# Performance work log

Measured on AMD Instinct MI355X. Metric: run time of the kernel, lower is better.

Reference implementation:

```python
import jax, jax.numpy as jnp
import numpy as np

FM = 256          # feature_maps
ROUNDS = 32
N_VARS = 4000
N_CLAUSES = 16800 # ~4.2 * n_vars (3-SAT phase transition)
K = 3             # literals per clause
EPS = 1e-8


def setup_inputs() -> dict:
    key = jax.random.key(0)
    ks = jax.random.split(key, 20)

    def nrm(k, shape):
        # tf.initializers.RandomNormal default stddev = 0.05
        return jax.random.normal(k, shape, jnp.float32) * 0.05

    vs = jax.random.randint(ks[0], (N_CLAUSES, K), 1, N_VARS + 1)
    sg = jnp.where(jax.random.uniform(ks[1], (N_CLAUSES, K)) < 0.5, -1, 1)
    return {
        "clause_lits": (vs * sg).astype(jnp.int32),  # signed 1-based literals
        "n_vars": N_VARS,
        "L_init": nrm(ks[2], (1, FM)), "C_init": nrm(ks[3], (1, FM)),
        "LC_W0": nrm(ks[4], (FM, FM)), "LC_b0": jnp.zeros((FM,), jnp.float32),
        "LC_W1": nrm(ks[5], (FM, FM)), "LC_b1": jnp.zeros((FM,), jnp.float32),
        "LC_W2": nrm(ks[6], (FM, FM)), "LC_b2": jnp.zeros((FM,), jnp.float32),
        "CL_W0": nrm(ks[7], (FM, FM)), "CL_b0": jnp.zeros((FM,), jnp.float32),
        "CL_W1": nrm(ks[8], (FM, FM)), "CL_b1": jnp.zeros((FM,), jnp.float32),
        "CL_W2": nrm(ks[9], (FM, FM)), "CL_b2": jnp.zeros((FM,), jnp.float32),
        "C_Wx": nrm(ks[10], (FM, 4 * FM)), "C_Wh": nrm(ks[11], (FM, 4 * FM)),
        "C_b": jnp.zeros((4 * FM,), jnp.float32),
        "L_Wx": nrm(ks[12], (2 * FM, 4 * FM)), "L_Wh": nrm(ks[13], (FM, 4 * FM)),
        "L_b": jnp.zeros((4 * FM,), jnp.float32),
        "V_W0": nrm(ks[14], (2 * FM, 2 * FM)), "V_b0": jnp.zeros((2 * FM,), jnp.float32),
        "V_W1": nrm(ks[15], (2 * FM, 2 * FM)), "V_b1": jnp.zeros((2 * FM,), jnp.float32),
        "V_W2": nrm(ks[16], (2 * FM, 1)), "V_b2": jnp.zeros((1,), jnp.float32),
    }


def _mlp3(x, W0, b0, W1, b1, W2, b2):
    h = jax.nn.relu(x @ W0 + b0)
    h = jax.nn.relu(h @ W1 + b1)
    return h @ W2 + b2


def _lstm(x, h, c, Wx, Wh, b):
    # keras LSTMCell: gate order i, f, g, o; sigmoid recurrent, tanh activation
    z = x @ Wx + h @ Wh + b
    i, f, g, o = jnp.split(z, 4, axis=1)
    c = jax.nn.sigmoid(f) * c + jax.nn.sigmoid(i) * jnp.tanh(g)
    h = jax.nn.sigmoid(o) * jnp.tanh(c)
    return h, c


def reference(clause_lits, n_vars, L_init, C_init,
              LC_W0, LC_b0, LC_W1, LC_b1, LC_W2, LC_b2,
              CL_W0, CL_b0, CL_W1, CL_b1, CL_W2, CL_b2,
              C_Wx, C_Wh, C_b, L_Wx, L_Wh, L_b,
              V_W0, V_b0, V_W1, V_b1, V_W2, V_b2):
    n_clauses = clause_lits.shape[0]
    n_lits = 2 * n_vars
    lits = clause_lits.reshape(-1)                         # [E]
    sign = jnp.sign(lits).astype(jnp.float32)              # [E]
    var_idx = jnp.abs(lits) - 1                            # [E] 0-based var
    lit_idx = jnp.where(lits > 0, var_idx, n_vars + var_idx)
    clause_idx = jnp.repeat(jnp.arange(n_clauses), clause_lits.shape[1])

    denom = jnp.sqrt(jnp.float32(FM))
    l_h = jnp.tile(L_init / denom, (n_lits, 1))
    c_h = jnp.tile(C_init / denom, (n_clauses, 1))
    l_c = jnp.zeros_like(l_h)
    c_c = jnp.zeros_like(c_h)

    def vote(lh):
        variables = jnp.concatenate([lh[:n_vars], lh[n_vars:]], axis=1)  # [n_vars, 2*FM]
        return _mlp3(variables, V_W0, V_b0, V_W1, V_b1, V_W2, V_b2)      # [n_vars, 1]

    def clause_loss(logits):
        # softplus_log_square_loss: clause_val = exp(-sum_lit softplus(sign*logit))
        vals = logits[var_idx, 0] * sign                   # [E]
        s = jax.ops.segment_sum(jax.nn.softplus(vals), clause_idx,
                                num_segments=n_clauses, indices_are_sorted=True)
        cv = jnp.exp(-s)
        return jnp.sum(jnp.square(-jnp.log(1.0 - cv + EPS)))

    def round_fn(carry, _):
        lh, lc, ch, cc, loss = carry
        lc_pre = _mlp3(lh, LC_W0, LC_b0, LC_W1, LC_b1, LC_W2, LC_b2)
        # SpMM adj^T @ msgs: scatter literal messages into clauses
        lc_msgs = jax.ops.segment_sum(lc_pre[lit_idx], clause_idx,
                                      num_segments=n_clauses, indices_are_sorted=True)
        ch, cc = _lstm(lc_msgs, ch, cc, C_Wx, C_Wh, C_b)
        cl_pre = _mlp3(ch, CL_W0, CL_b0, CL_W1, CL_b1, CL_W2, CL_b2)
        # SpMM adj @ msgs: scatter clause messages into literals
        cl_msgs = jax.ops.segment_sum(cl_pre[clause_idx], lit_idx, num_segments=n_lits)
        flipped = jnp.concatenate([lh[n_vars:], lh[:n_vars]], axis=0)
        lh, lc = _lstm(jnp.concatenate([cl_msgs, flipped], axis=1), lh, lc,
                       L_Wx, L_Wh, L_b)
        loss = loss + clause_loss(vote(lh))
        return (lh, lc, ch, cc, loss), None

    (l_h, l_c, c_h, c_c, loss), _ = jax.lax.scan(
        round_fn, (l_h, l_c, c_h, c_c, jnp.float32(0.0)), None, length=ROUNDS)
    logits = vote(l_h)
    return logits, loss / jnp.float32(ROUNDS)
```

## Files before the change

### kernel.cpp

```cpp
#include <hip/hip_runtime.h>
#include <hip/hip_bf16.h>

#define NV 4000
#define NL 8000
#define NC 16800
#define NE 50400
#define FM 256
#define ROUNDS 32

typedef short s16x8 __attribute__((ext_vector_type(8)));
typedef __bf16 b16x8 __attribute__((ext_vector_type(8)));
typedef float f32x4 __attribute__((ext_vector_type(4)));
union V8 { s16x8 s; b16x8 b; ushort u[8]; };

using gaddr_t = const void __attribute__((address_space(1)))*;
using laddr_t = void __attribute__((address_space(3)))*;

__device__ __forceinline__ float b2f(ushort u) {
    union { uint i; float f; } v; v.i = ((uint)u) << 16; return v.f;
}
__device__ __forceinline__ ushort f2b(float f) {
    __hip_bfloat16 h = __float2bfloat16(f);
    return *(ushort*)&h;
}

__global__ void zero_kernel(float* __restrict__ p, int n) {
    int i = blockIdx.x * blockDim.x + threadIdx.x;
    if (i < n) p[i] = 0.0f;
}
__global__ void f2b_kernel(const float* __restrict__ src, ushort* __restrict__ dst, int n) {
    int i = blockIdx.x * blockDim.x + threadIdx.x;
    if (i < n) dst[i] = f2b(src[i]);
}
__global__ void transpose_w_kernel(const float* __restrict__ in, ushort* __restrict__ out,
                                   int K, int N, int ldo, int koff, int perm) {
    int idx = blockIdx.x * blockDim.x + threadIdx.x;
    if (idx >= K * N) return;
    int n = idx / K, k = idx - n * K;
    int row = perm ? ((n & 255) * 4 + (n >> 8)) : n;
    out[(size_t)row * ldo + koff + k] = f2b(in[(size_t)k * N + n]);
}
__global__ void permute_bias_kernel(const float* __restrict__ b, float* __restrict__ bp) {
    int n = blockIdx.x * blockDim.x + threadIdx.x;
    if (n < 1024) bp[(n & 255) * 4 + (n >> 8)] = b[n];
}

__global__ void init_lh_kernel(const float* __restrict__ Li, ushort* __restrict__ lh,
                               ushort* __restrict__ lhflip) {
    int idx = blockIdx.x * blockDim.x + threadIdx.x;
    if (idx < NL * FM) {
        ushort v = f2b(Li[idx & (FM - 1)] * (1.0f / 16.0f));
        lh[idx] = v; lhflip[idx] = v;
    }
}
__global__ void init_ch_kernel(const float* __restrict__ Ci, ushort* __restrict__ ch) {
    int idx = blockIdx.x * blockDim.x + threadIdx.x;
    if (idx < NC * FM) ch[idx] = f2b(Ci[idx & (FM - 1)] * (1.0f / 16.0f));
}

__global__ void csr_count_kernel(const int* __restrict__ lits, int* __restrict__ deg) {
    int e = blockIdx.x * blockDim.x + threadIdx.x;
    if (e >= NE) return;
    int l = lits[e];
    int v = (l > 0 ? l : -l) - 1;
    int li = (l > 0) ? v : NV + v;
    atomicAdd(&deg[li], 1);
}
__global__ void csr_scan_kernel(const int* __restrict__ deg, int* __restrict__ rowptr,
                                int* __restrict__ nxt) {
    if (threadIdx.x == 0 && blockIdx.x == 0) {
        int acc = 0;
        for (int i = 0; i < NL; ++i) { rowptr[i] = acc; nxt[i] = acc; acc += deg[i]; }
        rowptr[NL] = acc;
    }
}
__global__ void csr_fill_kernel(const int* __restrict__ lits, int* __restrict__ nxt,
                                int* __restrict__ ecl) {
    int e = blockIdx.x * blockDim.x + threadIdx.x;
    if (e >= NE) return;
    int l = lits[e];
    int v = (l > 0 ? l : -l) - 1;
    int li = (l > 0) ? v : NV + v;
    int pos = atomicAdd(&nxt[li], 1);
    ecl[pos] = e / 3;
}

#define BKT 64

#define MLPR 32
__global__ __launch_bounds__(256) void mlp3_kernel(
    const ushort* __restrict__ A,
    const ushort* __restrict__ W0t, const float* __restrict__ b0,
    const ushort* __restrict__ W1t, const float* __restrict__ b1,
    const ushort* __restrict__ W2t, const float* __restrict__ b2,
    ushort* __restrict__ out, int M)
{
    __shared__ __align__(16) ushort As[MLPR * BKT];
    __shared__ __align__(16) ushort Wl[256 * BKT];
    __shared__ __align__(16) ushort Ab[MLPR * 264];
    const int tid = threadIdx.x;
    const int lane = tid & 63, wid = tid >> 6;
    const int rowBase = blockIdx.x * MLPR;
    const int lr = lane >> 3, ql = (lane & 7) ^ lr;
    const int cl16 = lane & 15, kg = lane >> 4;

    const ushort* Wt[3] = {W0t, W1t, W2t};
    const float*  bs[3] = {b0, b1, b2};

    #pragma unroll
    for (int layer = 0; layer < 3; ++layer) {
        f32x4 acc[2][4];
        #pragma unroll
        for (int i = 0; i < 2; ++i)
            #pragma unroll
            for (int j = 0; j < 4; ++j) acc[i][j] = (f32x4){0.f, 0.f, 0.f, 0.f};

        for (int kt = 0; kt < 4; ++kt) {
            __syncthreads();
            #pragma unroll
            for (int t = 0; t < 8; ++t) {
                int row = wid * 64 + t * 8 + lr;
                __builtin_amdgcn_global_load_lds(
                    (gaddr_t)(Wt[layer] + (size_t)row * 256 + kt * 64 + ql * 8),
                    (laddr_t)&Wl[(wid * 64 + t * 8) * BKT + lane * 8], 16, 0, 0);
            }
            if (layer == 0) {
                int row = rowBase + wid * 8 + lr;
                if (row > M - 1) row = M - 1;
                __builtin_amdgcn_global_load_lds(
                    (gaddr_t)(A + (size_t)row * 256 + kt * 64 + ql * 8),
                    (laddr_t)&As[wid * 512 + lane * 8], 16, 0, 0);
            }
            __syncthreads();
            #pragma unroll
            for (int s = 0; s < 2; ++s) {
                int kq8 = s * 4 + kg;
                V8 af[2], bf[4];
                #pragma unroll
                for (int i = 0; i < 2; ++i) {
                    int m = i * 16 + cl16;
                    if (layer == 0)
                        af[i].s = *(const s16x8*)&As[m * BKT + ((kq8 ^ (m & 7)) * 8)];
                    else
                        af[i].s = *(const s16x8*)&Ab[m * 264 + kt * 64 + kq8 * 8];
                }
                #pragma unroll
                for (int j = 0; j < 4; ++j) {
                    int n = wid * 64 + j * 16 + cl16;
                    bf[j].s = *(const s16x8*)&Wl[n * BKT + ((kq8 ^ (n & 7)) * 8)];
                }
                #pragma unroll
                for (int i = 0; i < 2; ++i)
                    #pragma unroll
                    for (int j = 0; j < 4; ++j)
                        acc[i][j] = __builtin_amdgcn_mfma_f32_16x16x32_bf16(
                            af[i].b, bf[j].b, acc[i][j], 0, 0, 0);
            }
        }
        __syncthreads();
        const int rq = (lane >> 4) * 4;
        #pragma unroll
        for (int i = 0; i < 2; ++i)
            #pragma unroll
            for (int r = 0; r < 4; ++r) {
                int row = i * 16 + rq + r;
                #pragma unroll
                for (int j = 0; j < 4; ++j) {
                    int col = wid * 64 + j * 16 + cl16;
                    float v = acc[i][j][r] + bs[layer][col];
                    if (layer < 2) {
                        Ab[row * 264 + col] = f2b(fmaxf(v, 0.0f));
                    } else {
                        int grow = rowBase + row;
                        if (grow < M) out[(size_t)grow * 256 + col] = f2b(v);
                    }
                }
            }
    }
}

__global__ __launch_bounds__(256) void gemm16_n64_kernel(
    const ushort* __restrict__ A0, int K0,
    const ushort* __restrict__ A1, int K1,
    const ushort* __restrict__ Bt, const float* __restrict__ bias,
    ushort* __restrict__ C, int M, int N, int relu)
{
    __shared__ __align__(16) ushort Al[128 * BKT];
    __shared__ __align__(16) ushort Bl[64 * BKT];
    const int Ktot = K0 + K1;
    const int tid = threadIdx.x;
    const int rowBase = blockIdx.y * 128, colBase = blockIdx.x * 64;
    const int lane = tid & 63, wid = tid >> 6;
    const int wm = (wid & 1) * 64, wn = (wid >> 1) * 32;
    const int lr = lane >> 3, ql = (lane & 7) ^ lr;

    f32x4 acc[4][2];
    #pragma unroll
    for (int i = 0; i < 4; ++i)
        #pragma unroll
        for (int j = 0; j < 2; ++j) acc[i][j] = (f32x4){0.f, 0.f, 0.f, 0.f};

    for (int k0 = 0; k0 < Ktot; k0 += BKT) {
        const ushort* As; int ks, lda;
        if (k0 < K0) { As = A0; ks = k0; lda = K0; }
        else         { As = A1; ks = k0 - K0; lda = K1; }
        __syncthreads();
        #pragma unroll
        for (int t = 0; t < 4; ++t) {
            int rloc = (wid * 4 + t) * 8 + lr;
            int ga = rowBase + rloc; if (ga > M - 1) ga = M - 1;
            __builtin_amdgcn_global_load_lds((gaddr_t)(As + (size_t)ga * lda + ks + ql * 8),
                                             (laddr_t)&Al[(wid * 4 + t) * 512], 16, 0, 0);
        }
        #pragma unroll
        for (int t = 0; t < 2; ++t) {
            int rloc = (wid * 2 + t) * 8 + lr;
            __builtin_amdgcn_global_load_lds((gaddr_t)(Bt + (size_t)(colBase + rloc) * Ktot + k0 + ql * 8),
                                             (laddr_t)&Bl[(wid * 2 + t) * 512], 16, 0, 0);
        }
        __syncthreads();
        const int cl = lane & 15, kg = lane >> 4;
        #pragma unroll
        for (int s = 0; s < 2; ++s) {
            V8 af[4], bf[2];
            #pragma unroll
            for (int i = 0; i < 4; ++i) {
                int m = wm + i * 16 + cl;
                af[i].s = *(const s16x8*)&Al[m * BKT + (((s * 4 + kg) ^ (m & 7)) * 8)];
            }
            #pragma unroll
            for (int j = 0; j < 2; ++j) {
                int n = wn + j * 16 + cl;
                bf[j].s = *(const s16x8*)&Bl[n * BKT + (((s * 4 + kg) ^ (n & 7)) * 8)];
            }
            #pragma unroll
            for (int i = 0; i < 4; ++i)
                #pragma unroll
                for (int j = 0; j < 2; ++j)
                    acc[i][j] = __builtin_amdgcn_mfma_f32_16x16x32_bf16(af[i].b, bf[j].b,
                                                                        acc[i][j], 0, 0, 0);
        }
    }
    const int rq = (lane >> 4) * 4, cl = lane & 15;
    #pragma unroll
    for (int i = 0; i < 4; ++i)
        #pragma unroll
        for (int r = 0; r < 4; ++r) {
            int grow = rowBase + wm + i * 16 + rq + r;
            if (grow >= M) continue;
            #pragma unroll
            for (int j = 0; j < 2; ++j) {
                int gcol = colBase + wn + j * 16 + cl;
                float v = acc[i][j][r] + bias[gcol];
                if (relu) v = fmaxf(v, 0.0f);
                C[(size_t)grow * N + gcol] = f2b(v);
            }
        }
}

__global__ __launch_bounds__(256) void gemm_lstm_kernel(
    const ushort* __restrict__ A0, int K0,
    const ushort* __restrict__ A1, int K1,
    const ushort* __restrict__ A2, int K2,
    const ushort* __restrict__ Bt, const float* __restrict__ biasP,
    float* __restrict__ c32, ushort* __restrict__ h_out,
    ushort* __restrict__ hflip_out, int M)
{
    __shared__ __align__(16) ushort smem[2 * 128 * BKT];
    ushort* Al = smem;
    ushort* Bl = smem + 128 * BKT;
    const int Ktot = K0 + K1 + K2;
    const int tid = threadIdx.x;
    const int rowBase = blockIdx.y * 128, colBase = blockIdx.x * 128;
    const int lane = tid & 63, wid = tid >> 6;
    const int wm = (wid >> 1) * 64, wn = (wid & 1) * 64;
    const int lr = lane >> 3, ql = (lane & 7) ^ lr;

    f32x4 acc[4][4];
    #pragma unroll
    for (int i = 0; i < 4; ++i)
        #pragma unroll
        for (int j = 0; j < 4; ++j) acc[i][j] = (f32x4){0.f, 0.f, 0.f, 0.f};

    for (int k0 = 0; k0 < Ktot; k0 += BKT) {
        const ushort* As; int ks, lda;
        if (k0 < K0)           { As = A0; ks = k0;           lda = K0; }
        else if (k0 < K0 + K1) { As = A1; ks = k0 - K0;      lda = K1; }
        else                   { As = A2; ks = k0 - K0 - K1; lda = K2; }
        __syncthreads();
        #pragma unroll
        for (int t = 0; t < 4; ++t) {
            int rloc = (wid * 4 + t) * 8 + lr;
            int ga = rowBase + rloc; if (ga > M - 1) ga = M - 1;
            __builtin_amdgcn_global_load_lds((gaddr_t)(As + (size_t)ga * lda + ks + ql * 8),
                                             (laddr_t)&Al[(wid * 4 + t) * 512], 16, 0, 0);
            __builtin_amdgcn_global_load_lds((gaddr_t)(Bt + (size_t)(colBase + rloc) * Ktot + k0 + ql * 8),
                                             (laddr_t)&Bl[(wid * 4 + t) * 512], 16, 0, 0);
        }
        __syncthreads();
        const int cl = lane & 15, kg = lane >> 4;
        #pragma unroll
        for (int s = 0; s < 2; ++s) {
            V8 af[4], bf[4];
            #pragma unroll
            for (int i = 0; i < 4; ++i) {
                int m = wm + i * 16 + cl;
                af[i].s = *(const s16x8*)&Al[m * BKT + (((s * 4 + kg) ^ (m & 7)) * 8)];
            }
            #pragma unroll
            for (int j = 0; j < 4; ++j) {
                int n = wn + j * 16 + cl;
                bf[j].s = *(const s16x8*)&Bl[n * BKT + (((s * 4 + kg) ^ (n & 7)) * 8)];
            }
            #pragma unroll
            for (int i = 0; i < 4; ++i)
                #pragma unroll
                for (int j = 0; j < 4; ++j)
                    acc[i][j] = __builtin_amdgcn_mfma_f32_16x16x32_bf16(af[i].b, bf[j].b,
                                                                        acc[i][j], 0, 0, 0);
        }
    }
    __syncthreads();
    {
        const int rq = (lane >> 4) * 4, cl = lane & 15;
        #pragma unroll
        for (int i = 0; i < 4; ++i)
            #pragma unroll
            for (int r = 0; r < 4; ++r) {
                int rl = wm + i * 16 + rq + r;
                #pragma unroll
                for (int j = 0; j < 4; ++j) {
                    int clc = wn + j * 16 + cl;
                    smem[rl * 128 + clc] = f2b(acc[i][j][r] + biasP[colBase + clc]);
                }
            }
    }
    __syncthreads();
    const int fl = tid & 31, rg = tid >> 5;
    const int fglob = (colBase >> 2) + fl;
    #pragma unroll
    for (int k = 0; k < 16; ++k) {
        int rl = rg + 8 * k;
        int grow = rowBase + rl;
        if (grow >= M) continue;
        ushort4 g4 = *(const ushort4*)&smem[rl * 128 + fl * 4];
        float zi = b2f(g4.x), zf = b2f(g4.y), zg = b2f(g4.z), zo = b2f(g4.w);
        size_t ci = (size_t)grow * FM + fglob;
        float cold = c32[ci];
        float si = 1.0f / (1.0f + __expf(-zi));
        float sf = 1.0f / (1.0f + __expf(-zf));
        float so = 1.0f / (1.0f + __expf(-zo));
        float cn = sf * cold + si * tanhf(zg);
        float hn = so * tanhf(cn);
        c32[ci] = cn;
        ushort hb = f2b(hn);
        h_out[ci] = hb;
        if (hflip_out) hflip_out[(size_t)((grow + NV) % NL) * FM + fglob] = hb;
    }
}

__global__ void gather_lc8_kernel(const ushort* __restrict__ pre, const int* __restrict__ lits,
                                  ushort* __restrict__ out) {
    int idx = blockIdx.x * blockDim.x + threadIdx.x;
    if (idx >= NC * 32) return;
    int c = idx >> 5, f8 = (idx & 31) * 8;
    const int* cl = lits + c * 3;
    float s[8] = {};
    #pragma unroll
    for (int k = 0; k < 3; ++k) {
        int l = cl[k];
        int v = (l > 0 ? l : -l) - 1;
        int li = (l > 0) ? v : NV + v;
        V8 x; x.s = *(const s16x8*)&pre[(size_t)li * FM + f8];
        #pragma unroll
        for (int e = 0; e < 8; ++e) s[e] += b2f(x.u[e]);
    }
    V8 o;
    #pragma unroll
    for (int e = 0; e < 8; ++e) o.u[e] = f2b(s[e]);
    *(s16x8*)&out[(size_t)c * FM + f8] = o.s;
}

__global__ void gather_cl8_kernel(const ushort* __restrict__ pre, const int* __restrict__ rowptr,
                                  const int* __restrict__ ecl, ushort* __restrict__ out) {
    int idx = blockIdx.x * blockDim.x + threadIdx.x;
    if (idx >= NL * 32) return;
    int li = idx >> 5, f8 = (idx & 31) * 8;
    int j0 = rowptr[li], j1 = rowptr[li + 1];
    float s[8] = {};
    for (int j = j0; j < j1; ++j) {
        V8 x; x.s = *(const s16x8*)&pre[(size_t)ecl[j] * FM + f8];
        #pragma unroll
        for (int e = 0; e < 8; ++e) s[e] += b2f(x.u[e]);
    }
    V8 o;
    #pragma unroll
    for (int e = 0; e < 8; ++e) o.u[e] = f2b(s[e]);
    *(s16x8*)&out[(size_t)li * FM + f8] = o.s;
}

__global__ void vote_out_kernel(const ushort* __restrict__ h1, const ushort* __restrict__ w,
                                const float* __restrict__ b, float* __restrict__ logits_hist,
                                float* __restrict__ out_f32) {
    int gtid = blockIdx.x * blockDim.x + threadIdx.x;
    int wid = gtid >> 6;
    int lane = threadIdx.x & 63;
    if (wid >= NV) return;
    const ushort* hr = h1 + (size_t)wid * 512;
    float s = 0.0f;
    #pragma unroll
    for (int k = 0; k < 8; ++k) s += b2f(hr[lane + 64 * k]) * b2f(w[lane + 64 * k]);
    #pragma unroll
    for (int off = 32; off; off >>= 1) s += __shfl_down(s, off);
    if (lane == 0) {
        float v = s + b[0];
        logits_hist[wid] = v;
        out_f32[wid] = v;
    }
}

__global__ __launch_bounds__(256) void loss_all_kernel(
    const float* __restrict__ logits_hist, const int* __restrict__ lits,
    float* __restrict__ loss_arr)
{
    __shared__ float sm[256];
    const int r = blockIdx.y;
    const float* logits = logits_hist + (size_t)r * NV;
    int c = blockIdx.x * 256 + threadIdx.x;
    float t2 = 0.0f;
    if (c < NC) {
        const int* cl = lits + c * 3;
        float s = 0.0f;
        #pragma unroll
        for (int k = 0; k < 3; ++k) {
            int l = cl[k];
            int v = (l > 0 ? l : -l) - 1;
            float sg = (l > 0) ? 1.0f : -1.0f;
            float val = logits[v] * sg;
            s += fmaxf(val, 0.0f) + log1pf(__expf(-fabsf(val)));
        }
        float cv = __expf(-s);
        float t = -logf(1.0f - cv + 1e-8f);
        t2 = t * t;
    }
    sm[threadIdx.x] = t2;
    __syncthreads();
    for (int st = 128; st > 0; st >>= 1) {
        if (threadIdx.x < st) sm[threadIdx.x] += sm[threadIdx.x + st];
        __syncthreads();
    }
    if (threadIdx.x == 0) atomicAdd(&loss_arr[r], sm[0]);
}

__global__ void final_loss_kernel(const float* __restrict__ loss_arr, float* __restrict__ out) {
    if (threadIdx.x == 0 && blockIdx.x == 0) {
        float s = 0.0f;
        for (int r = 0; r < ROUNDS; ++r) s += loss_arr[r];
        out[NV] = s * (1.0f / (float)ROUNDS);
    }
}

extern "C" void kernel_launch(void* const* d_in, const int* in_sizes, int n_in,
                              void* d_out, int out_size, void* d_ws, size_t ws_size,
                              hipStream_t stream) {
    const int* lits = (const int*)d_in[0];
    float* out = (float*)d_out;

    const float* Li   = (const float*)d_in[2];
    const float* Ci   = (const float*)d_in[3];
    const float* LCW0 = (const float*)d_in[4];
    const float* LCb0 = (const float*)d_in[5];
    const float* LCW1 = (const float*)d_in[6];
    const float* LCb1 = (const float*)d_in[7];
    const float* LCW2 = (const float*)d_in[8];
    const float* LCb2 = (const float*)d_in[9];
    const float* CLW0 = (const float*)d_in[10];
    const float* CLb0 = (const float*)d_in[11];
    const float* CLW1 = (const float*)d_in[12];
    const float* CLb1 = (const float*)d_in[13];
    const float* CLW2 = (const float*)d_in[14];
    const float* CLb2 = (const float*)d_in[15];
    const float* CWx  = (const float*)d_in[16];
    const float* CWh  = (const float*)d_in[17];
    const float* Cb   = (const float*)d_in[18];
    const float* LWx  = (const float*)d_in[19];
    const float* LWh  = (const float*)d_in[20];
    const float* Lb   = (const float*)d_in[21];
    const float* VW0  = (const float*)d_in[22];
    const float* Vb0  = (const float*)d_in[23];
    const float* VW1  = (const float*)d_in[24];
    const float* Vb1  = (const float*)d_in[25];
    const float* VW2  = (const float*)d_in[26];
    const float* Vb2  = (const float*)d_in[27];
    (void)in_sizes; (void)n_in; (void)out_size; (void)ws_size;

    char* base = (char*)d_ws;
    size_t off = 0;
    auto allocB = [&](size_t bytes) {
        void* p = base + off;
        off += (bytes + 15) & ~(size_t)15;
        return p;
    };
    float*  loss_arr    = (float*)allocB(ROUNDS * 4);
    float*  logits_hist = (float*)allocB((size_t)ROUNDS * NV * 4);
    float*  lc32        = (float*)allocB((size_t)NL * FM * 4);
    float*  cc32        = (float*)allocB((size_t)NC * FM * 4);
    float*  Cb_p        = (float*)allocB(1024 * 4);
    float*  Lb_p        = (float*)allocB(1024 * 4);
    int*    deg         = (int*)allocB(NL * 4);
    int*    rowptr      = (int*)allocB((NL + 1) * 4);
    int*    nxt         = (int*)allocB(NL * 4);
    int*    ecl         = (int*)allocB(NE * 4);
    ushort* LC0t = (ushort*)allocB((size_t)256 * 256 * 2);
    ushort* LC1t = (ushort*)allocB((size_t)256 * 256 * 2);
    ushort* LC2t = (ushort*)allocB((size_t)256 * 256 * 2);
    ushort* CL0t = (ushort*)allocB((size_t)256 * 256 * 2);
    ushort* CL1t = (ushort*)allocB((size_t)256 * 256 * 2);
    ushort* CL2t = (ushort*)allocB((size_t)256 * 256 * 2);
    ushort* CWt  = (ushort*)allocB((size_t)1024 * 512 * 2);
    ushort* LWt  = (ushort*)allocB((size_t)1024 * 768 * 2);
    ushort* VW0t = (ushort*)allocB((size_t)512 * 512 * 2);
    ushort* VW1t = (ushort*)allocB((size_t)512 * 512 * 2);
    ushort* vw2  = (ushort*)allocB((size_t)512 * 2);
    ushort* lh_a = (ushort*)allocB((size_t)NL * FM * 2);
    ushort* lh_b = (ushort*)allocB((size_t)NL * FM * 2);
    ushort* lf_a = (ushort*)allocB((size_t)NL * FM * 2);
    ushort* lf_b = (ushort*)allocB((size_t)NL * FM * 2);
    ushort* ch_a = (ushort*)allocB((size_t)NC * FM * 2);
    ushort* ch_b = (ushort*)allocB((size_t)NC * FM * 2);
    ushort* lcm16 = (ushort*)allocB((size_t)NC * FM * 2);
    ushort* clm16 = (ushort*)allocB((size_t)NL * FM * 2);
    ushort* tL    = (ushort*)allocB((size_t)NL * FM * 2);
    ushort* tC    = (ushort*)allocB((size_t)NC * FM * 2);
    ushort* v0    = (ushort*)allocB((size_t)NV * 512 * 2);
    ushort* v1    = (ushort*)allocB((size_t)NV * 512 * 2);

    auto tw = [&](const float* in, ushort* o, int K, int N, int ldo, int koff, int perm) {
        hipLaunchKernelGGL(transpose_w_kernel, dim3((K * N + 255) / 256), dim3(256), 0, stream,
                           in, o, K, N, ldo, koff, perm);
    };
    tw(LCW0, LC0t, 256, 256, 256, 0, 0);
    tw(LCW1, LC1t, 256, 256, 256, 0, 0);
    tw(LCW2, LC2t, 256, 256, 256, 0, 0);
    tw(CLW0, CL0t, 256, 256, 256, 0, 0);
    tw(CLW1, CL1t, 256, 256, 256, 0, 0);
    tw(CLW2, CL2t, 256, 256, 256, 0, 0);
    tw(CWx,  CWt, 256, 1024, 512, 0, 1);
    tw(CWh,  CWt, 256, 1024, 512, 256, 1);
    tw(LWx,  LWt, 512, 1024, 768, 0, 1);
    tw(LWh,  LWt, 256, 1024, 768, 512, 1);
    tw(VW0,  VW0t, 512, 512, 512, 0, 0);
    tw(VW1,  VW1t, 512, 512, 512, 0, 0);
    hipLaunchKernelGGL(f2b_kernel, dim3(2), dim3(256), 0, stream, VW2, vw2, 512);
    hipLaunchKernelGGL(permute_bias_kernel, dim3(4), dim3(256), 0, stream, Cb, Cb_p);
    hipLaunchKernelGGL(permute_bias_kernel, dim3(4), dim3(256), 0, stream, Lb, Lb_p);

    hipLaunchKernelGGL(init_lh_kernel, dim3(NL * FM / 256), dim3(256), 0, stream, Li, lh_a, lf_a);
    hipLaunchKernelGGL(init_ch_kernel, dim3(NC * FM / 256), dim3(256), 0, stream, Ci, ch_a);
    hipLaunchKernelGGL(zero_kernel, dim3(NL * FM / 256), dim3(256), 0, stream, lc32, NL * FM);
    hipLaunchKernelGGL(zero_kernel, dim3(NC * FM / 256), dim3(256), 0, stream, cc32, NC * FM);
    hipLaunchKernelGGL(zero_kernel, dim3(1), dim3(256), 0, stream, loss_arr, ROUNDS);
    hipLaunchKernelGGL(zero_kernel, dim3((NL + 255) / 256), dim3(256), 0, stream, (float*)deg, NL);
    hipLaunchKernelGGL(csr_count_kernel, dim3((NE + 255) / 256), dim3(256), 0, stream, lits, deg);
    hipLaunchKernelGGL(csr_scan_kernel, dim3(1), dim3(64), 0, stream, deg, rowptr, nxt);
    hipLaunchKernelGGL(csr_fill_kernel, dim3((NE + 255) / 256), dim3(256), 0, stream, lits, nxt, ecl);

    auto gemm64 = [&](const ushort* A0, int K0, const ushort* A1, int K1,
                      const ushort* Bt, const float* bias, ushort* C, int M, int N, int relu) {
        hipLaunchKernelGGL(gemm16_n64_kernel, dim3(N / 64, (M + 127) / 128), dim3(256), 0, stream,
                           A0, K0, A1, K1, Bt, bias, C, M, N, relu);
    };

    ushort *lh_c = lh_a, *lh_n = lh_b, *lf_c = lf_a, *lf_n = lf_b, *ch_c = ch_a, *ch_n = ch_b;

    for (int r = 0; r < ROUNDS; ++r) {
        hipLaunchKernelGGL(mlp3_kernel, dim3(NL / MLPR), dim3(256), 0, stream,
                           lh_c, LC0t, LCb0, LC1t, LCb1, LC2t, LCb2, tL, NL);
        hipLaunchKernelGGL(gather_lc8_kernel, dim3(NC * 32 / 256), dim3(256), 0, stream,
                           tL, lits, lcm16);
        hipLaunchKernelGGL(gemm_lstm_kernel, dim3(8, (NC + 127) / 128), dim3(256), 0, stream,
                           lcm16, 256, ch_c, 256, (const ushort*)0, 0,
                           CWt, Cb_p, cc32, ch_n, (ushort*)0, NC);
        hipLaunchKernelGGL(mlp3_kernel, dim3(NC / MLPR, 1), dim3(256), 0, stream,
                           ch_n, CL0t, CLb0, CL1t, CLb1, CL2t, CLb2, tC, NC);
        hipLaunchKernelGGL(gather_cl8_kernel, dim3(NL * 32 / 256), dim3(256), 0, stream,
                           tC, rowptr, ecl, clm16);
        hipLaunchKernelGGL(gemm_lstm_kernel, dim3(8, (NL + 127) / 128), dim3(256), 0, stream,
                           clm16, 256, lf_c, 256, lh_c, 256,
                           LWt, Lb_p, lc32, lh_n, lf_n, NL);
        gemm64(lh_n, 256, lh_n + (size_t)NV * FM, 256, VW0t, Vb0, v0, NV, 512, 1);
        gemm64(v0, 512, 0, 0, VW1t, Vb1, v1, NV, 512, 1);
        hipLaunchKernelGGL(vote_out_kernel, dim3(NV * 64 / 256), dim3(256), 0, stream,
                           v1, vw2, Vb2, logits_hist + (size_t)r * NV, out);
        ushort* tswap;
        tswap = lh_c; lh_c = lh_n; lh_n = tswap;
        tswap = lf_c; lf_c = lf_n; lf_n = tswap;
        tswap = ch_c; ch_c = ch_n; ch_n = tswap;
    }

    hipLaunchKernelGGL(loss_all_kernel, dim3((NC + 255) / 256, ROUNDS), dim3(256), 0, stream,
                       logits_hist, lits, loss_arr);
    hipLaunchKernelGGL(final_loss_kernel, dim3(1), dim3(64), 0, stream, loss_arr, out);
}
```

Baseline: 5.781 ms.

## Fuse vote MLP into one kernel and read flipped hidden state by index remap

Replaces the two vote GEMM launches and the dot-product kernel with one fused kernel that keeps the first hidden layer in LDS and reduces the final dot product in-block. The literal LSTM GEMM now loads the flipped hidden rows by remapping row indices instead of reading a separately written flipped copy, removing that buffer and its scattered writes. The fused kernel uses only 125 blocks, and each block re-streams both 512x512 weight matrices, which reduces parallelism and adds weight traffic.

```diff
diff --git a/kernel.cpp b/kernel.cpp
--- a/kernel.cpp
+++ b/kernel.cpp
@@ -45,13 +45,9 @@
     if (n < 1024) bp[(n & 255) * 4 + (n >> 8)] = b[n];
 }
 
-__global__ void init_lh_kernel(const float* __restrict__ Li, ushort* __restrict__ lh,
-                               ushort* __restrict__ lhflip) {
+__global__ void init_lh_kernel(const float* __restrict__ Li, ushort* __restrict__ lh) {
     int idx = blockIdx.x * blockDim.x + threadIdx.x;
-    if (idx < NL * FM) {
-        ushort v = f2b(Li[idx & (FM - 1)] * (1.0f / 16.0f));
-        lh[idx] = v; lhflip[idx] = v;
-    }
+    if (idx < NL * FM) lh[idx] = f2b(Li[idx & (FM - 1)] * (1.0f / 16.0f));
 }
 __global__ void init_ch_kernel(const float* __restrict__ Ci, ushort* __restrict__ ch) {
     int idx = blockIdx.x * blockDim.x + threadIdx.x;
@@ -179,92 +175,13 @@
     }
 }
 
-__global__ __launch_bounds__(256) void gemm16_n64_kernel(
-    const ushort* __restrict__ A0, int K0,
-    const ushort* __restrict__ A1, int K1,
-    const ushort* __restrict__ Bt, const float* __restrict__ bias,
-    ushort* __restrict__ C, int M, int N, int relu)
-{
-    __shared__ __align__(16) ushort Al[128 * BKT];
-    __shared__ __align__(16) ushort Bl[64 * BKT];
-    const int Ktot = K0 + K1;
-    const int tid = threadIdx.x;
-    const int rowBase = blockIdx.y * 128, colBase = blockIdx.x * 64;
-    const int lane = tid & 63, wid = tid >> 6;
-    const int wm = (wid & 1) * 64, wn = (wid >> 1) * 32;
-    const int lr = lane >> 3, ql = (lane & 7) ^ lr;
-
-    f32x4 acc[4][2];
-    #pragma unroll
-    for (int i = 0; i < 4; ++i)
-        #pragma unroll
-        for (int j = 0; j < 2; ++j) acc[i][j] = (f32x4){0.f, 0.f, 0.f, 0.f};
-
-    for (int k0 = 0; k0 < Ktot; k0 += BKT) {
-        const ushort* As; int ks, lda;
-        if (k0 < K0) { As = A0; ks = k0; lda = K0; }
-        else         { As = A1; ks = k0 - K0; lda = K1; }
-        __syncthreads();
-        #pragma unroll
-        for (int t = 0; t < 4; ++t) {
-            int rloc = (wid * 4 + t) * 8 + lr;
-            int ga = rowBase + rloc; if (ga > M - 1) ga = M - 1;
-            __builtin_amdgcn_global_load_lds((gaddr_t)(As + (size_t)ga * lda + ks + ql * 8),
-                                             (laddr_t)&Al[(wid * 4 + t) * 512], 16, 0, 0);
-        }
-        #pragma unroll
-        for (int t = 0; t < 2; ++t) {
-            int rloc = (wid * 2 + t) * 8 + lr;
-            __builtin_amdgcn_global_load_lds((gaddr_t)(Bt + (size_t)(colBase + rloc) * Ktot + k0 + ql * 8),
-                                             (laddr_t)&Bl[(wid * 2 + t) * 512], 16, 0, 0);
-        }
-        __syncthreads();
-        const int cl = lane & 15, kg = lane >> 4;
-        #pragma unroll
-        for (int s = 0; s < 2; ++s) {
-            V8 af[4], bf[2];
-            #pragma unroll
-            for (int i = 0; i < 4; ++i) {
-                int m = wm + i * 16 + cl;
-                af[i].s = *(const s16x8*)&Al[m * BKT + (((s * 4 + kg) ^ (m & 7)) * 8)];
-            }
-            #pragma unroll
-            for (int j = 0; j < 2; ++j) {
-                int n = wn + j * 16 + cl;
-                bf[j].s = *(const s16x8*)&Bl[n * BKT + (((s * 4 + kg) ^ (n & 7)) * 8)];
-            }
-            #pragma unroll
-            for (int i = 0; i < 4; ++i)
-                #pragma unroll
-                for (int j = 0; j < 2; ++j)
-                    acc[i][j] = __builtin_amdgcn_mfma_f32_16x16x32_bf16(af[i].b, bf[j].b,
-                                                                        acc[i][j], 0, 0, 0);
-        }
-    }
-    const int rq = (lane >> 4) * 4, cl = lane & 15;
-    #pragma unroll
-    for (int i = 0; i < 4; ++i)
-        #pragma unroll
-        for (int r = 0; r < 4; ++r) {
-            int grow = rowBase + wm + i * 16 + rq + r;
-            if (grow >= M) continue;
-            #pragma unroll
-            for (int j = 0; j < 2; ++j) {
-                int gcol = colBase + wn + j * 16 + cl;
-                float v = acc[i][j][r] + bias[gcol];
-                if (relu) v = fmaxf(v, 0.0f);
-                C[(size_t)grow * N + gcol] = f2b(v);
-            }
-        }
-}
-
 __global__ __launch_bounds__(256) void gemm_lstm_kernel(
     const ushort* __restrict__ A0, int K0,
     const ushort* __restrict__ A1, int K1,
     const ushort* __restrict__ A2, int K2,
+    int flip1,
     const ushort* __restrict__ Bt, const float* __restrict__ biasP,
-    float* __restrict__ c32, ushort* __restrict__ h_out,
-    ushort* __restrict__ hflip_out, int M)
+    float* __restrict__ c32, ushort* __restrict__ h_out, int M)
 {
     __shared__ __align__(16) ushort smem[2 * 128 * BKT];
     ushort* Al = smem;
@@ -283,15 +200,16 @@
         for (int j = 0; j < 4; ++j) acc[i][j] = (f32x4){0.f, 0.f, 0.f, 0.f};
 
     for (int k0 = 0; k0 < Ktot; k0 += BKT) {
-        const ushort* As; int ks, lda;
-        if (k0 < K0)           { As = A0; ks = k0;           lda = K0; }
-        else if (k0 < K0 + K1) { As = A1; ks = k0 - K0;      lda = K1; }
-        else                   { As = A2; ks = k0 - K0 - K1; lda = K2; }
+        const ushort* As; int ks, lda, flip;
+        if (k0 < K0)           { As = A0; ks = k0;           lda = K0; flip = 0; }
+        else if (k0 < K0 + K1) { As = A1; ks = k0 - K0;      lda = K1; flip = flip1; }
+        else                   { As = A2; ks = k0 - K0 - K1; lda = K2; flip = 0; }
         __syncthreads();
         #pragma unroll
         for (int t = 0; t < 4; ++t) {
             int rloc = (wid * 4 + t) * 8 + lr;
             int ga = rowBase + rloc; if (ga > M - 1) ga = M - 1;
+            if (flip) ga = (ga < NV) ? ga + NV : ga - NV;
             __builtin_amdgcn_global_load_lds((gaddr_t)(As + (size_t)ga * lda + ks + ql * 8),
                                              (laddr_t)&Al[(wid * 4 + t) * 512], 16, 0, 0);
             __builtin_amdgcn_global_load_lds((gaddr_t)(Bt + (size_t)(colBase + rloc) * Ktot + k0 + ql * 8),
@@ -353,9 +271,153 @@
         float cn = sf * cold + si * tanhf(zg);
         float hn = so * tanhf(cn);
         c32[ci] = cn;
-        ushort hb = f2b(hn);
-        h_out[ci] = hb;
-        if (hflip_out) hflip_out[(size_t)((grow + NV) % NL) * FM + fglob] = hb;
+        h_out[ci] = f2b(hn);
+    }
+}
+
+#define VR 32
+__global__ __launch_bounds__(256) void vote_fused_kernel(
+    const ushort* __restrict__ lh,
+    const ushort* __restrict__ W0t, const float* __restrict__ b0,
+    const ushort* __restrict__ W1t, const float* __restrict__ b1,
+    const ushort* __restrict__ w2,  const float* __restrict__ b2,
+    float* __restrict__ logits_hist, float* __restrict__ out_f32)
+{
+    __shared__ __align__(16) ushort As[VR * BKT];
+    __shared__ __align__(16) ushort Wl[256 * BKT];
+    __shared__ __align__(16) ushort Ab[VR * 520];
+    __shared__ float pl[VR];
+    const int tid = threadIdx.x;
+    const int lane = tid & 63, wid = tid >> 6;
+    const int rowBase = blockIdx.x * VR;
+    const int lr = lane >> 3, ql = (lane & 7) ^ lr;
+    const int cl16 = lane & 15, kg = lane >> 4;
+    if (tid < VR) pl[tid] = 0.0f;
+
+    for (int half = 0; half < 2; ++half) {
+        f32x4 acc[2][4];
+        #pragma unroll
+        for (int i = 0; i < 2; ++i)
+            #pragma unroll
+            for (int j = 0; j < 4; ++j) acc[i][j] = (f32x4){0.f, 0.f, 0.f, 0.f};
+        for (int kt = 0; kt < 8; ++kt) {
+            __syncthreads();
+            #pragma unroll
+            for (int t = 0; t < 8; ++t) {
+                int row = half * 256 + wid * 64 + t * 8 + lr;
+                __builtin_amdgcn_global_load_lds(
+                    (gaddr_t)(W0t + (size_t)row * 512 + kt * 64 + ql * 8),
+                    (laddr_t)&Wl[(wid * 64 + t * 8) * BKT + lane * 8], 16, 0, 0);
+            }
+            {
+                int v = rowBase + wid * 8 + lr;
+                int k = kt * 64;
+                const ushort* src = (k < 256) ? (lh + (size_t)v * 256 + k)
+                                              : (lh + (size_t)(v + NV) * 256 + (k - 256));
+                __builtin_amdgcn_global_load_lds((gaddr_t)(src + ql * 8),
+                                                 (laddr_t)&As[wid * 512 + lane * 8], 16, 0, 0);
+            }
+            __syncthreads();
+            #pragma unroll
+            for (int s = 0; s < 2; ++s) {
+                int kq8 = s * 4 + kg;
+                V8 af[2], bf[4];
+                #pragma unroll
+                for (int i = 0; i < 2; ++i) {
+                    int m = i * 16 + cl16;
+                    af[i].s = *(const s16x8*)&As[m * BKT + ((kq8 ^ (m & 7)) * 8)];
+                }
+                #pragma unroll
+                for (int j = 0; j < 4; ++j) {
+                    int n = wid * 64 + j * 16 + cl16;
+                    bf[j].s = *(const s16x8*)&Wl[n * BKT + ((kq8 ^ (n & 7)) * 8)];
+                }
+                #pragma unroll
+                for (int i = 0; i < 2; ++i)
+                    #pragma unroll
+                    for (int j = 0; j < 4; ++j)
+                        acc[i][j] = __builtin_amdgcn_mfma_f32_16x16x32_bf16(
+                            af[i].b, bf[j].b, acc[i][j], 0, 0, 0);
+            }
+        }
+        __syncthreads();
+        const int rq = (lane >> 4) * 4;
+        #pragma unroll
+        for (int i = 0; i < 2; ++i)
+            #pragma unroll
+            for (int r = 0; r < 4; ++r) {
+                int row = i * 16 + rq + r;
+                #pragma unroll
+                for (int j = 0; j < 4; ++j) {
+                    int col = half * 256 + wid * 64 + j * 16 + cl16;
+                    float v = acc[i][j][r] + b0[col];
+                    Ab[row * 520 + col] = f2b(fmaxf(v, 0.0f));
+                }
+            }
+    }
+    for (int half = 0; half < 2; ++half) {
+        f32x4 acc[2][4];
+        #pragma unroll
+        for (int i = 0; i < 2; ++i)
+            #pragma unroll
+            for (int j = 0; j < 4; ++j) acc[i][j] = (f32x4){0.f, 0.f, 0.f, 0.f};
+        for (int kt = 0; kt < 8; ++kt) {
+            __syncthreads();
+            #pragma unroll
+            for (int t = 0; t < 8; ++t) {
+                int row = half * 256 + wid * 64 + t * 8 + lr;
+                __builtin_amdgcn_global_load_lds(
+                    (gaddr_t)(W1t + (size_t)row * 512 + kt * 64 + ql * 8),
+                    (laddr_t)&Wl[(wid * 64 + t * 8) * BKT + lane * 8], 16, 0, 0);
+            }
+            __syncthreads();
+            #pragma unroll
+            for (int s = 0; s < 2; ++s) {
+                int kq8 = s * 4 + kg;
+                V8 af[2], bf[4];
+                #pragma unroll
+                for (int i = 0; i < 2; ++i) {
+                    int m = i * 16 + cl16;
+                    af[i].s = *(const s16x8*)&Ab[m * 520 + kt * 64 + kq8 * 8];
+                }
+                #pragma unroll
+                for (int j = 0; j < 4; ++j) {
+                    int n = wid * 64 + j * 16 + cl16;
+                    bf[j].s = *(const s16x8*)&Wl[n * BKT + ((kq8 ^ (n & 7)) * 8)];
+                }
+                #pragma unroll
+                for (int i = 0; i < 2; ++i)
+                    #pragma unroll
+                    for (int j = 0; j < 4; ++j)
+                        acc[i][j] = __builtin_amdgcn_mfma_f32_16x16x32_bf16(
+                            af[i].b, bf[j].b, acc[i][j], 0, 0, 0);
+            }
+        }
+        const int rq = (lane >> 4) * 4;
+        #pragma unroll
+        for (int i = 0; i < 2; ++i)
+            #pragma unroll
+            for (int r = 0; r < 4; ++r) {
+                float s = 0.0f;
+                #pragma unroll
+                for (int j = 0; j < 4; ++j) {
+                    int col = half * 256 + wid * 64 + j * 16 + cl16;
+                    float h1 = b2f(f2b(fmaxf(acc[i][j][r] + b1[col], 0.0f)));
+                    s += h1 * b2f(w2[col]);
+                }
+                s += __shfl_xor(s, 1);
+                s += __shfl_xor(s, 2);
+                s += __shfl_xor(s, 4);
+                s += __shfl_xor(s, 8);
+                if (cl16 == 0) atomicAdd(&pl[i * 16 + rq + r], s);
+            }
+    }
+    __syncthreads();
+    if (tid < VR) {
+        int grow = rowBase + tid;
+        float v = pl[tid] + b2[0];
+        logits_hist[grow] = v;
+        out_f32[grow] = v;
     }
 }
 
@@ -397,26 +459,6 @@
     #pragma unroll
     for (int e = 0; e < 8; ++e) o.u[e] = f2b(s[e]);
     *(s16x8*)&out[(size_t)li * FM + f8] = o.s;
-}
-
-__global__ void vote_out_kernel(const ushort* __restrict__ h1, const ushort* __restrict__ w,
-                                const float* __restrict__ b, float* __restrict__ logits_hist,
-                                float* __restrict__ out_f32) {
-    int gtid = blockIdx.x * blockDim.x + threadIdx.x;
-    int wid = gtid >> 6;
-    int lane = threadIdx.x & 63;
-    if (wid >= NV) return;
-    const ushort* hr = h1 + (size_t)wid * 512;
-    float s = 0.0f;
-    #pragma unroll
-    for (int k = 0; k < 8; ++k) s += b2f(hr[lane + 64 * k]) * b2f(w[lane + 64 * k]);
-    #pragma unroll
-    for (int off = 32; off; off >>= 1) s += __shfl_down(s, off);
-    if (lane == 0) {
-        float v = s + b[0];
-        logits_hist[wid] = v;
-        out_f32[wid] = v;
-    }
 }
 
 __global__ __launch_bounds__(256) void loss_all_kernel(
@@ -524,16 +566,12 @@
     ushort* vw2  = (ushort*)allocB((size_t)512 * 2);
     ushort* lh_a = (ushort*)allocB((size_t)NL * FM * 2);
     ushort* lh_b = (ushort*)allocB((size_t)NL * FM * 2);
-    ushort* lf_a = (ushort*)allocB((size_t)NL * FM * 2);
-    ushort* lf_b = (ushort*)allocB((size_t)NL * FM * 2);
     ushort* ch_a = (ushort*)allocB((size_t)NC * FM * 2);
     ushort* ch_b = (ushort*)allocB((size_t)NC * FM * 2);
     ushort* lcm16 = (ushort*)allocB((size_t)NC * FM * 2);
     ushort* clm16 = (ushort*)allocB((size_t)NL * FM * 2);
     ushort* tL    = (ushort*)allocB((size_t)NL * FM * 2);
     ushort* tC    = (ushort*)allocB((size_t)NC * FM * 2);
-    ushort* v0    = (ushort*)allocB((size_t)NV * 512 * 2);
-    ushort* v1    = (ushort*)allocB((size_t)NV * 512 * 2);
 
     auto tw = [&](const float* in, ushort* o, int K, int N, int ldo, int koff, int perm) {
         hipLaunchKernelGGL(transpose_w_kernel, dim3((K * N + 255) / 256), dim3(256), 0, stream,
@@ -555,7 +593,7 @@
     hipLaunchKernelGGL(permute_bias_kernel, dim3(4), dim3(256), 0, stream, Cb, Cb_p);
     hipLaunchKernelGGL(permute_bias_kernel, dim3(4), dim3(256), 0, stream, Lb, Lb_p);
 
-    hipLaunchKernelGGL(init_lh_kernel, dim3(NL * FM / 256), dim3(256), 0, stream, Li, lh_a, lf_a);
+    hipLaunchKernelGGL(init_lh_kernel, dim3(NL * FM / 256), dim3(256), 0, stream, Li, lh_a);
     hipLaunchKernelGGL(init_ch_kernel, dim3(NC * FM / 256), dim3(256), 0, stream, Ci, ch_a);
     hipLaunchKernelGGL(zero_kernel, dim3(NL * FM / 256), dim3(256), 0, stream, lc32, NL * FM);
     hipLaunchKernelGGL(zero_kernel, dim3(NC * FM / 256), dim3(256), 0, stream, cc32, NC * FM);
@@ -565,13 +603,7 @@
     hipLaunchKernelGGL(csr_scan_kernel, dim3(1), dim3(64), 0, stream, deg, rowptr, nxt);
     hipLaunchKernelGGL(csr_fill_kernel, dim3((NE + 255) / 256), dim3(256), 0, stream, lits, nxt, ecl);
 
-    auto gemm64 = [&](const ushort* A0, int K0, const ushort* A1, int K1,
-                      const ushort* Bt, const float* bias, ushort* C, int M, int N, int relu) {
-        hipLaunchKernelGGL(gemm16_n64_kernel, dim3(N / 64, (M + 127) / 128), dim3(256), 0, stream,
-                           A0, K0, A1, K1, Bt, bias, C, M, N, relu);
-    };
-
-    ushort *lh_c = lh_a, *lh_n = lh_b, *lf_c = lf_a, *lf_n = lf_b, *ch_c = ch_a, *ch_n = ch_b;
+    ushort *lh_c = lh_a, *lh_n = lh_b, *ch_c = ch_a, *ch_n = ch_b;
 
     for (int r = 0; r < ROUNDS; ++r) {
         hipLaunchKernelGGL(mlp3_kernel, dim3(NL / MLPR), dim3(256), 0, stream,
@@ -579,22 +611,20 @@
         hipLaunchKernelGGL(gather_lc8_kernel, dim3(NC * 32 / 256), dim3(256), 0, stream,
                            tL, lits, lcm16);
         hipLaunchKernelGGL(gemm_lstm_kernel, dim3(8, (NC + 127) / 128), dim3(256), 0, stream,
-                           lcm16, 256, ch_c, 256, (const ushort*)0, 0,
-                           CWt, Cb_p, cc32, ch_n, (ushort*)0, NC);
+                           lcm16, 256, ch_c, 256, (const ushort*)0, 0, 0,
+                           CWt, Cb_p, cc32, ch_n, NC);
         hipLaunchKernelGGL(mlp3_kernel, dim3(NC / MLPR, 1), dim3(256), 0, stream,
                            ch_n, CL0t, CLb0, CL1t, CLb1, CL2t, CLb2, tC, NC);
         hipLaunchKernelGGL(gather_cl8_kernel, dim3(NL * 32 / 256), dim3(256), 0, stream,
                            tC, rowptr, ecl, clm16);
         hipLaunchKernelGGL(gemm_lstm_kernel, dim3(8, (NL + 127) / 128), dim3(256), 0, stream,
-                           clm16, 256, lf_c, 256, lh_c, 256,
-                           LWt, Lb_p, lc32, lh_n, lf_n, NL);
-        gemm64(lh_n, 256, lh_n + (size_t)NV * FM, 256, VW0t, Vb0, v0, NV, 512, 1);
-        gemm64(v0, 512, 0, 0, VW1t, Vb1, v1, NV, 512, 1);
-        hipLaunchKernelGGL(vote_out_kernel, dim3(NV * 64 / 256), dim3(256), 0, stream,
-                           v1, vw2, Vb2, logits_hist + (size_t)r * NV, out);
+                           clm16, 256, lh_c, 256, lh_c, 256, 1,
+                           LWt, Lb_p, lc32, lh_n, NL);
+        hipLaunchKernelGGL(vote_fused_kernel, dim3(NV / VR), dim3(256), 0, stream,
+                           lh_n, VW0t, Vb0, VW1t, Vb1, vw2, Vb2,
+                           logits_hist + (size_t)r * NV, out);
         ushort* tswap;
         tswap = lh_c; lh_c = lh_n; lh_n = tswap;
-        tswap = lf_c; lf_c = lf_n; lf_n = tswap;
         tswap = ch_c; ch_c = ch_n; ch_n = tswap;
     }
 
```

After: 5.896 ms. Within noise of the previous version (+2.0%).
